# Kernel optimization log

Hardware: AMD Instinct MI355X
Metric: run time of the kernel (lower is better)

Reference implementation:

```python
import jax, jax.numpy as jnp
import numpy as np

B, D, H, E, TOP_K = 16384, 256, 1024, 8, 2


def setup_inputs() -> dict:
    key = jax.random.key(0)
    ks = jax.random.split(key, 12)
    s = 0.02
    return {
        "t": jax.random.uniform(ks[0], (B,), dtype=jnp.float32),
        "x": jax.random.normal(ks[1], (B, D), dtype=jnp.float32),
        # router: Linear(D+1,H) -> SiLU -> Linear(H,E)
        "Rw1": jax.random.normal(ks[2], (D + 1, H), dtype=jnp.float32) * s,
        "Rb1": jnp.zeros((H,), dtype=jnp.float32),
        "Rw2": jax.random.normal(ks[3], (H, E), dtype=jnp.float32) * s,
        "Rb2": jnp.zeros((E,), dtype=jnp.float32),
        # stacked expert MLPs: (D+1)->H->H->D for each of E experts
        "Ew1": jax.random.normal(ks[4], (E, D + 1, H), dtype=jnp.float32) * s,
        "Eb1": jnp.zeros((E, H), dtype=jnp.float32),
        "Ew2": jax.random.normal(ks[5], (E, H, H), dtype=jnp.float32) * s,
        "Eb2": jnp.zeros((E, H), dtype=jnp.float32),
        "Ew3": jax.random.normal(ks[6], (E, H, D), dtype=jnp.float32) * s,
        "Eb3": jnp.zeros((E, D), dtype=jnp.float32),
    }


def reference(t, x, Rw1, Rb1, Rw2, Rb2, Ew1, Eb1, Ew2, Eb2, Ew3, Eb3):
    t_vec = t.reshape(-1, 1)                      # (B,1)
    xt = jnp.concatenate([x, t_vec], axis=-1)     # (B,D+1)

    # router logits
    h = jax.nn.silu(xt @ Rw1 + Rb1)
    logits = h @ Rw2 + Rb2                        # (B,E)

    # top-k sparse gating (top_k < num_experts)
    topk_vals, topk_idx = jax.lax.top_k(logits, TOP_K)
    mask = jnp.zeros_like(logits).at[jnp.arange(logits.shape[0])[:, None], topk_idx].set(1.0)
    masked_logits = jnp.where(mask == 0, -jnp.inf, logits)
    alpha = jax.nn.softmax(masked_logits, axis=-1)  # (B,E)

    # dense all-expert MLPs (faithful to the original stack+einsum)
    h1 = jax.nn.silu(jnp.einsum('bi,eih->beh', xt, Ew1) + Eb1)   # (B,E,H)
    h2 = jax.nn.silu(jnp.einsum('beh,ehg->beg', h1, Ew2) + Eb2)  # (B,E,H)
    expert_out = jnp.einsum('beh,ehd->bed', h2, Ew3) + Eb3       # (B,E,D)

    velocity = jnp.einsum('be,bed->bd', alpha, expert_out)       # (B,D)
    return velocity
```

## Files before the change

kernel.cpp:

```cpp
#include <hip/hip_runtime.h>
#include <cstdint>
#include <cstddef>

#define NB   16384
#define DD   256
#define DIN  257
#define KP1  288
#define HH   1024
#define NE   8
#define GMAX 33792
#define GMT  264

#define CTRL_INTS 272

typedef unsigned short u16;
typedef __bf16 bf16x8 __attribute__((ext_vector_type(8)));
typedef float  f32x4  __attribute__((ext_vector_type(4)));
typedef unsigned short u16x4 __attribute__((ext_vector_type(4)));

__device__ __forceinline__ u16 f2bf(float f) {
  union { float f; unsigned u; } v; v.f = f;
  return (u16)((v.u + 0x7FFFu + ((v.u >> 16) & 1u)) >> 16);
}
__device__ __forceinline__ float bf2f(u16 h) {
  union { unsigned u; float f; } v; v.u = ((unsigned)h) << 16;
  return v.f;
}

#define GLDS16(g, l) __builtin_amdgcn_global_load_lds( \
    (const __attribute__((address_space(1))) void*)(g), \
    (__attribute__((address_space(3))) void*)(l), 16, 0, 0)

__device__ __forceinline__ int swz_u16(int row, int q) {
  return row * 32 + ((q ^ ((row >> 1) & 3)) * 8);
}

__global__ void build_xt3(const float* __restrict__ x, const float* __restrict__ t,
                          u16* __restrict__ xh, u16* __restrict__ xm, u16* __restrict__ xl) {
  long i = (long)blockIdx.x * 256 + threadIdx.x;
  int b = (int)(i / 72), qd = (int)(i % 72);
  f32x4 v;
  if (qd < 64)       v = *(const f32x4*)&x[(long)b * DD + qd * 4];
  else if (qd == 64) v = (f32x4){t[b], 0.f, 0.f, 0.f};
  else               v = (f32x4){0.f, 0.f, 0.f, 0.f};
  u16x4 h, m, l;
  #pragma unroll
  for (int j = 0; j < 4; ++j) {
    u16 hi = f2bf(v[j]);  float r1 = v[j] - bf2f(hi);
    u16 mi = f2bf(r1);    float r2 = r1 - bf2f(mi);
    h[j] = hi; m[j] = mi; l[j] = f2bf(r2);
  }
  long o = (long)b * KP1 + qd * 4;
  *(u16x4*)&xh[o] = h;  *(u16x4*)&xm[o] = m;  *(u16x4*)&xl[o] = l;
}

__global__ void transpose_all(const float* __restrict__ Rw1, const float* __restrict__ Ew1,
                              const float* __restrict__ Ew2, const float* __restrict__ Ew3,
                              u16* __restrict__ R1h, u16* __restrict__ R1m, u16* __restrict__ R1l,
                              u16* __restrict__ E1t, u16* __restrict__ E2t, u16* __restrict__ E3t) {
  __shared__ float tile[32][33];
  int bid = blockIdx.x;
  const float* W; u16 *Wh, *Wm = nullptr, *Wl = nullptr;
  int Kdim, Ndim, Kpad, e = 0, kt, nt;
  long sW = 0, sWt = 0;
  if (bid < 288) {
    kt = bid % 9; nt = bid / 9;
    W = Rw1; Wh = R1h; Wm = R1m; Wl = R1l; Kdim = DIN; Ndim = HH; Kpad = KP1;
  } else if (bid < 2592) {
    int b = bid - 288; e = b / 288; b %= 288; kt = b % 9; nt = b / 9;
    W = Ew1; Wh = E1t; Kdim = DIN; Ndim = HH; Kpad = KP1; sW = (long)DIN * HH; sWt = (long)HH * KP1;
  } else if (bid < 10784) {
    int b = bid - 2592; e = b / 1024; b %= 1024; kt = b % 32; nt = b / 32;
    W = Ew2; Wh = E2t; Kdim = HH; Ndim = HH; Kpad = HH; sW = (long)HH * HH; sWt = (long)HH * HH;
  } else {
    int b = bid - 10784; e = b / 256; b %= 256; kt = b % 32; nt = b / 32;
    W = Ew3; Wh = E3t; Kdim = HH; Ndim = DD; Kpad = HH; sW = (long)HH * DD; sWt = (long)DD * HH;
  }
  int k0 = kt * 32, n0 = nt * 32;
  int tx = threadIdx.x, ty = threadIdx.y;
  const float* Wb = W + (long)e * sW;
  #pragma unroll
  for (int i = 0; i < 4; ++i) {
    int k = k0 + ty + i * 8;
    tile[ty + i * 8][tx] = (k < Kdim) ? Wb[(long)k * Ndim + (n0 + tx)] : 0.f;
  }
  __syncthreads();
  #pragma unroll
  for (int i = 0; i < 4; ++i) {
    int n = n0 + ty + i * 8;
    float v = tile[tx][ty + i * 8];
    long o = (long)e * sWt + (long)n * Kpad + k0 + tx;
    u16 hi = f2bf(v);
    Wh[o] = hi;
    if (Wm) {
      float r1 = v - bf2f(hi);
      u16 mi = f2bf(r1);
      Wm[o] = mi;
      Wl[o] = f2bf(r1 - bf2f(mi));
    }
  }
}

__global__ __launch_bounds__(256, 2)
void router_gemm_emul3(const u16* __restrict__ Ah, const u16* __restrict__ Am, const u16* __restrict__ Al,
                       const u16* __restrict__ Bh, const u16* __restrict__ Bm, const u16* __restrict__ Bl,
                       const float* __restrict__ bias, const float* __restrict__ Rw2,
                       float* __restrict__ pbuf) {
  __shared__ __align__(16) u16 S[6][128 * 32];
  int tid = threadIdx.x;
  int bid = blockIdx.x;
  int xcd = bid & 7, j = bid >> 3;
  int mt = (j >> 3) * 8 + xcd, nt = j & 7;
  int m0 = mt * 128, n0 = nt * 128;
  const u16* Ap[3] = {Ah, Am, Al};
  const u16* Bp[3] = {Bh, Bm, Bl};
  const u16 *ag[3][2], *bg[3][2];
  u16 *la[3][2], *lb[3][2];
  #pragma unroll
  for (int r = 0; r < 2; ++r) {
    int i = r * 256 + tid;
    int row = i >> 2;
    int qa = (i & 3) ^ ((row >> 1) & 3);
    int kq = qa * 8;
    #pragma unroll
    for (int p = 0; p < 3; ++p) {
      ag[p][r] = Ap[p] + (long)(m0 + row) * KP1 + kq;
      bg[p][r] = Bp[p] + (long)(n0 + row) * KP1 + kq;
      la[p][r] = &S[p][i * 8];
      lb[p][r] = &S[3 + p][i * 8];
    }
  }
  int lane = tid & 63, wv = tid >> 6;
  int wm = wv >> 1, wn = wv & 1;
  int q = lane >> 4, c = lane & 15;
  int offA[4], offB[4];
  #pragma unroll
  for (int t4 = 0; t4 < 4; ++t4) {
    offA[t4] = swz_u16(wm * 64 + t4 * 16 + c, q);
    offB[t4] = swz_u16(wn * 64 + t4 * 16 + c, q);
  }
  f32x4 acc[4][4];
  #pragma unroll
  for (int mi = 0; mi < 4; ++mi)
    #pragma unroll
    for (int ni = 0; ni < 4; ++ni) acc[mi][ni] = (f32x4){0.f, 0.f, 0.f, 0.f};

  for (int k0 = 0; k0 < KP1; k0 += 32) {
    __syncthreads();
    #pragma unroll
    for (int r = 0; r < 2; ++r)
      #pragma unroll
      for (int p = 0; p < 3; ++p) {
        GLDS16(ag[p][r] + k0, la[p][r]);
        GLDS16(bg[p][r] + k0, lb[p][r]);
      }
    __syncthreads();
    bf16x8 av[3][4], bv[3][4];
    #pragma unroll
    for (int mi = 0; mi < 4; ++mi)
      #pragma unroll
      for (int p = 0; p < 3; ++p) av[p][mi] = *(const bf16x8*)&S[p][offA[mi]];
    #pragma unroll
    for (int ni = 0; ni < 4; ++ni)
      #pragma unroll
      for (int p = 0; p < 3; ++p) bv[p][ni] = *(const bf16x8*)&S[3 + p][offB[ni]];
    #pragma unroll
    for (int mi = 0; mi < 4; ++mi)
      #pragma unroll
      for (int ni = 0; ni < 4; ++ni) {
        acc[mi][ni] = __builtin_amdgcn_mfma_f32_16x16x32_bf16(av[0][mi], bv[0][ni], acc[mi][ni], 0, 0, 0);
        acc[mi][ni] = __builtin_amdgcn_mfma_f32_16x16x32_bf16(av[0][mi], bv[1][ni], acc[mi][ni], 0, 0, 0);
        acc[mi][ni] = __builtin_amdgcn_mfma_f32_16x16x32_bf16(av[1][mi], bv[0][ni], acc[mi][ni], 0, 0, 0);
        acc[mi][ni] = __builtin_amdgcn_mfma_f32_16x16x32_bf16(av[0][mi], bv[2][ni], acc[mi][ni], 0, 0, 0);
        acc[mi][ni] = __builtin_amdgcn_mfma_f32_16x16x32_bf16(av[2][mi], bv[0][ni], acc[mi][ni], 0, 0, 0);
      }
  }
  float rw2f[4][8];
  #pragma unroll
  for (int ni = 0; ni < 4; ++ni) {
    const float* p = Rw2 + (long)(n0 + wn * 64 + ni * 16 + c) * NE;
    f32x4 a = *(const f32x4*)p, b2 = *(const f32x4*)(p + 4);
    #pragma unroll
    for (int j2 = 0; j2 < 4; ++j2) { rw2f[ni][j2] = a[j2]; rw2f[ni][4 + j2] = b2[j2]; }
  }
  float bi[4];
  #pragma unroll
  for (int ni = 0; ni < 4; ++ni) bi[ni] = bias[n0 + wn * 64 + ni * 16 + c];
  #pragma unroll
  for (int mi = 0; mi < 4; ++mi)
    #pragma unroll
    for (int r = 0; r < 4; ++r) {
      int token = m0 + wm * 64 + mi * 16 + q * 4 + r;
      float part[8] = {0.f, 0.f, 0.f, 0.f, 0.f, 0.f, 0.f, 0.f};
      #pragma unroll
      for (int ni = 0; ni < 4; ++ni) {
        float v = acc[mi][ni][r] + bi[ni];
        v = v / (1.f + expf(-v));
        #pragma unroll
        for (int e = 0; e < 8; ++e) part[e] += v * rw2f[ni][e];
      }
      #pragma unroll
      for (int m = 1; m < 16; m <<= 1)
        #pragma unroll
        for (int e = 0; e < 8; ++e) part[e] += __shfl_xor(part[e], m, 64);
      if (c == 0) {
        float* dst = pbuf + ((long)(nt * 2 + wn) * NB + token) * 8;
        *(f32x4*)dst       = (f32x4){part[0], part[1], part[2], part[3]};
        *(f32x4*)(dst + 4) = (f32x4){part[4], part[5], part[6], part[7]};
      }
    }
}

__global__ void reduce_topk(const float* __restrict__ pbuf, const float* __restrict__ Rb2,
                            int* __restrict__ tk_idx, float* __restrict__ tk_alpha,
                            int* __restrict__ ctrl) {
  __shared__ int lh[NE];
  int tid = threadIdx.x;
  if (tid < NE) lh[tid] = 0;
  __syncthreads();
  int token = blockIdx.x * 256 + tid;
  float v[8];
  #pragma unroll
  for (int e = 0; e < 8; ++e) v[e] = Rb2[e];
  #pragma unroll
  for (int p = 0; p < 16; ++p) {
    const float* src = pbuf + ((long)p * NB + token) * 8;
    f32x4 a = *(const f32x4*)src, b = *(const f32x4*)(src + 4);
    #pragma unroll
    for (int j = 0; j < 4; ++j) { v[j] += a[j]; v[4 + j] += b[j]; }
  }
  int i0 = 0;
  #pragma unroll
  for (int e = 1; e < NE; ++e) if (v[e] > v[i0]) i0 = e;
  int i1 = -1;
  #pragma unroll
  for (int e = 0; e < NE; ++e) { if (e == i0) continue; if (i1 < 0 || v[e] > v[i1]) i1 = e; }
  float d  = v[i1] - v[i0];
  float e1 = expf(d);
  float a0 = 1.f / (1.f + e1);
  float a1 = e1 / (1.f + e1);
  tk_idx[token * 2]     = i0;  tk_idx[token * 2 + 1]   = i1;
  tk_alpha[token * 2]   = a0;  tk_alpha[token * 2 + 1] = a1;
  atomicAdd(&lh[i0], 1);  atomicAdd(&lh[i1], 1);
  __syncthreads();
  if (tid < NE) atomicAdd(&ctrl[tid * 16], lh[tid]);
  __syncthreads();
  if (tid == 0) {
    __threadfence();
    int done = atomicAdd(&ctrl[270], 1);
    if (done == gridDim.x - 1) {
      int total = 0;
      for (int e = 0; e < NE; ++e) {
        ctrl[256 + e] = total;
        total += (atomicAdd(&ctrl[e * 16], 0) + 127) & ~127;
      }
      ctrl[256 + NE] = total;
    }
  }
}

__global__ void build_rowmap(const int* __restrict__ tk_idx, int* __restrict__ ctrl,
                             int* __restrict__ grow, int* __restrict__ tok2slot) {
  __shared__ int lh[NE];
  __shared__ int gb[NE];
  int tid = threadIdx.x;
  if (tid < NE) lh[tid] = 0;
  __syncthreads();
  int token = blockIdx.x * 256 + tid;
  int e0 = tk_idx[token * 2], e1 = tk_idx[token * 2 + 1];
  int l0 = atomicAdd(&lh[e0], 1);
  int l1 = atomicAdd(&lh[e1], 1);
  __syncthreads();
  if (tid < NE) gb[tid] = atomicAdd(&ctrl[128 + tid * 16], lh[tid]);
  __syncthreads();
  int g0 = ctrl[256 + e0] + gb[e0] + l0;
  int g1 = ctrl[256 + e1] + gb[e1] + l1;
  grow[g0] = token;  grow[g1] = token;
  tok2slot[token * 2] = g0;  tok2slot[token * 2 + 1] = g1;
}

template<int NKT, int NT, int MINW, bool GATHER, bool SILU, bool OUTF32>
__global__ __launch_bounds__(256, MINW)
void gemm_grouped(const u16* __restrict__ A, int lda,
                  const u16* __restrict__ Wt, long wstride, int ldw,
                  const float* __restrict__ bias, int bstride,
                  u16* __restrict__ C, int ldc,
                  float* __restrict__ Out, int ldo,
                  const int* __restrict__ offp,
                  const int* __restrict__ grow,
                  int K) {
  int bid = blockIdx.x;
  int xcd = bid & 7, j = bid >> 3;
  int mt = (j / NT) * 8 + xcd, nt = j % NT;
  int m0 = mt * 128, n0 = nt * 128;
  if (m0 >= offp[NE]) return;
  int e = 0;
  while (m0 >= offp[e + 1]) ++e;
  __shared__ __align__(16) u16 As[NKT][128 * 32];
  __shared__ __align__(16) u16 Bs[NKT][128 * 32];
  int tid = threadIdx.x;
  const u16 *ag[NKT][2], *bg[NKT][2];
  u16 *la[NKT][2], *lb[NKT][2];
  #pragma unroll
  for (int s = 0; s < NKT; ++s)
    #pragma unroll
    for (int r = 0; r < 2; ++r) {
      int i = r * 256 + tid;
      int row = i >> 2;
      int qa = (i & 3) ^ ((row >> 1) & 3);
      int kq = qa * 8 + s * 32;
      long arow = m0 + row;
      if (GATHER) arow = grow[arow];
      ag[s][r] = A + arow * lda + kq;
      bg[s][r] = Wt + (long)e * wstride + (long)(n0 + row) * ldw + kq;
      la[s][r] = &As[s][i * 8];
      lb[s][r] = &Bs[s][i * 8];
    }
  int lane = tid & 63, wv = tid >> 6;
  int wm = wv >> 1, wn = wv & 1;
  int q = lane >> 4, c = lane & 15;
  int offA[4], offB[4];
  #pragma unroll
  for (int t4 = 0; t4 < 4; ++t4) {
    offA[t4] = swz_u16(wm * 64 + t4 * 16 + c, q);
    offB[t4] = swz_u16(wn * 64 + t4 * 16 + c, q);
  }
  f32x4 acc[4][4];
  #pragma unroll
  for (int mi = 0; mi < 4; ++mi)
    #pragma unroll
    for (int ni = 0; ni < 4; ++ni) acc[mi][ni] = (f32x4){0.f, 0.f, 0.f, 0.f};

  for (int k0 = 0; k0 < K; k0 += 32 * NKT) {
    __syncthreads();
    #pragma unroll
    for (int s = 0; s < NKT; ++s)
      #pragma unroll
      for (int r = 0; r < 2; ++r) {
        GLDS16(ag[s][r] + k0, la[s][r]);
        GLDS16(bg[s][r] + k0, lb[s][r]);
      }
    __syncthreads();
    #pragma unroll
    for (int s = 0; s < NKT; ++s) {
      bf16x8 av[4], bv[4];
      #pragma unroll
      for (int mi = 0; mi < 4; ++mi)
        av[mi] = *(const bf16x8*)&As[s][offA[mi]];
      #pragma unroll
      for (int ni = 0; ni < 4; ++ni)
        bv[ni] = *(const bf16x8*)&Bs[s][offB[ni]];
      #pragma unroll
      for (int mi = 0; mi < 4; ++mi)
        #pragma unroll
        for (int ni = 0; ni < 4; ++ni)
          acc[mi][ni] = __builtin_amdgcn_mfma_f32_16x16x32_bf16(av[mi], bv[ni], acc[mi][ni], 0, 0, 0);
    }
  }
  #pragma unroll
  for (int mi = 0; mi < 4; ++mi)
    #pragma unroll
    for (int r = 0; r < 4; ++r) {
      int row = wm * 64 + mi * 16 + q * 4 + r;
      #pragma unroll
      for (int ni = 0; ni < 4; ++ni) {
        int col = n0 + wn * 64 + ni * 16 + c;
        float v = acc[mi][ni][r] + bias[e * bstride + col];
        if constexpr (SILU) v = v / (1.f + __expf(-v));
        if constexpr (OUTF32) {
          Out[(long)(m0 + row) * ldo + col] = v;
        } else {
          C[(long)(m0 + row) * ldc + col] = f2bf(v);
        }
      }
    }
}

__global__ void combine_out(const float* __restrict__ eo, const int* __restrict__ tok2slot,
                            const float* __restrict__ tk_alpha, float* __restrict__ out) {
  int i = blockIdx.x * 256 + threadIdx.x;
  int token = i >> 6, c4 = (i & 63) * 4;
  long s0 = tok2slot[token * 2], s1 = tok2slot[token * 2 + 1];
  float a0 = tk_alpha[token * 2], a1 = tk_alpha[token * 2 + 1];
  f32x4 v0 = *(const f32x4*)&eo[s0 * DD + c4];
  f32x4 v1 = *(const f32x4*)&eo[s1 * DD + c4];
  f32x4 r;
  #pragma unroll
  for (int j = 0; j < 4; ++j) r[j] = a0 * v0[j] + a1 * v1[j];
  *(f32x4*)&out[(long)token * DD + c4] = r;
}

extern "C" void kernel_launch(void* const* d_in, const int* in_sizes, int n_in,
                              void* d_out, int out_size, void* d_ws, size_t ws_size,
                              hipStream_t stream) {
  const float* t   = (const float*)d_in[0];
  const float* x   = (const float*)d_in[1];
  const float* Rw1 = (const float*)d_in[2];
  const float* Rb1 = (const float*)d_in[3];
  const float* Rw2 = (const float*)d_in[4];
  const float* Rb2 = (const float*)d_in[5];
  const float* Ew1 = (const float*)d_in[6];
  const float* Eb1 = (const float*)d_in[7];
  const float* Ew2 = (const float*)d_in[8];
  const float* Eb2 = (const float*)d_in[9];
  const float* Ew3 = (const float*)d_in[10];
  const float* Eb3 = (const float*)d_in[11];
  float* out = (float*)d_out;

  char* w = (char*)d_ws;
  size_t off = 0;
  auto alloc = [&](size_t bytes) { char* p = w + off; off = (off + bytes + 255) & ~(size_t)255; return p; };
  int*   ctrl     = (int*)  alloc(CTRL_INTS * 4);
  int*   grow     = (int*)  alloc((size_t)GMAX * 4);
  size_t zero_end = off;
  int*   tok2slot = (int*)  alloc((size_t)NB * 2 * 4);
  int*   tk_idx   = (int*)  alloc((size_t)NB * 2 * 4);
  float* tk_alpha = (float*)alloc((size_t)NB * 2 * 4);
  float* pbuf     = (float*)alloc((size_t)16 * NB * 8 * 4);
  u16* xh  = (u16*)alloc((size_t)NB * KP1 * 2);
  u16* xm  = (u16*)alloc((size_t)NB * KP1 * 2);
  u16* xl  = (u16*)alloc((size_t)NB * KP1 * 2);
  u16* R1h = (u16*)alloc((size_t)HH * KP1 * 2);
  u16* R1m = (u16*)alloc((size_t)HH * KP1 * 2);
  u16* R1l = (u16*)alloc((size_t)HH * KP1 * 2);
  u16* E1t = (u16*)alloc((size_t)NE * HH * KP1 * 2);
  u16* E2t = (u16*)alloc((size_t)NE * HH * HH * 2);
  u16* E3t = (u16*)alloc((size_t)NE * DD * HH * 2);
  u16* H1  = (u16*)alloc((size_t)GMAX * HH * 2);
  u16* H2  = (u16*)alloc((size_t)GMAX * HH * 2);
  float* eo = (float*)H1;

  hipMemsetAsync(d_ws, 0, zero_end, stream);

  build_xt3<<<(NB * 72) / 256, 256, 0, stream>>>(x, t, xh, xm, xl);
  transpose_all<<<12832, dim3(32, 8), 0, stream>>>(Rw1, Ew1, Ew2, Ew3,
                                                   R1h, R1m, R1l, E1t, E2t, E3t);

  router_gemm_emul3<<<(NB / 128) * 8, 256, 0, stream>>>(xh, xm, xl, R1h, R1m, R1l, Rb1, Rw2, pbuf);
  reduce_topk<<<NB / 256, 256, 0, stream>>>(pbuf, Rb2, tk_idx, tk_alpha, ctrl);
  build_rowmap<<<NB / 256, 256, 0, stream>>>(tk_idx, ctrl, grow, tok2slot);

  const int* offp = ctrl + 256;
  gemm_grouped<3, 8, 3, true, true, false><<<GMT * 8, 256, 0, stream>>>(
      xh, KP1, E1t, (long)HH * KP1, KP1, Eb1, HH, H1, HH, nullptr, 0, offp, grow, KP1);
  gemm_grouped<2, 8, 4, false, true, false><<<GMT * 8, 256, 0, stream>>>(
      H1, HH, E2t, (long)HH * HH, HH, Eb2, HH, H2, HH, nullptr, 0, offp, nullptr, HH);
  gemm_grouped<2, 2, 4, false, false, true><<<GMT * 2, 256, 0, stream>>>(
      H2, HH, E3t, (long)DD * HH, HH, Eb3, DD, nullptr, 0, eo, DD, offp, nullptr, HH);
  combine_out<<<(NB * DD / 4) / 256, 256, 0, stream>>>(eo, tok2slot, tk_alpha, out);
}
```

Measured before the change: 398.6 us.

## Fuse preprocessing kernels, split-K the final expert GEMM, parallelize top-k reduction

```diff
diff --git a/kernel.cpp b/kernel.cpp
--- a/kernel.cpp
+++ b/kernel.cpp
@@ -35,31 +35,35 @@
   return row * 32 + ((q ^ ((row >> 1) & 3)) * 8);
 }
 
-__global__ void build_xt3(const float* __restrict__ x, const float* __restrict__ t,
-                          u16* __restrict__ xh, u16* __restrict__ xm, u16* __restrict__ xl) {
-  long i = (long)blockIdx.x * 256 + threadIdx.x;
-  int b = (int)(i / 72), qd = (int)(i % 72);
-  f32x4 v;
-  if (qd < 64)       v = *(const f32x4*)&x[(long)b * DD + qd * 4];
-  else if (qd == 64) v = (f32x4){t[b], 0.f, 0.f, 0.f};
-  else               v = (f32x4){0.f, 0.f, 0.f, 0.f};
-  u16x4 h, m, l;
-  #pragma unroll
-  for (int j = 0; j < 4; ++j) {
-    u16 hi = f2bf(v[j]);  float r1 = v[j] - bf2f(hi);
-    u16 mi = f2bf(r1);    float r2 = r1 - bf2f(mi);
-    h[j] = hi; m[j] = mi; l[j] = f2bf(r2);
-  }
-  long o = (long)b * KP1 + qd * 4;
-  *(u16x4*)&xh[o] = h;  *(u16x4*)&xm[o] = m;  *(u16x4*)&xl[o] = l;
-}
-
-__global__ void transpose_all(const float* __restrict__ Rw1, const float* __restrict__ Ew1,
-                              const float* __restrict__ Ew2, const float* __restrict__ Ew3,
-                              u16* __restrict__ R1h, u16* __restrict__ R1m, u16* __restrict__ R1l,
-                              u16* __restrict__ E1t, u16* __restrict__ E2t, u16* __restrict__ E3t) {
+#define XT_BLOCKS 4608
+__global__ void preprocess(const float* __restrict__ x, const float* __restrict__ t,
+                           u16* __restrict__ xh, u16* __restrict__ xm, u16* __restrict__ xl,
+                           const float* __restrict__ Rw1, const float* __restrict__ Ew1,
+                           const float* __restrict__ Ew2, const float* __restrict__ Ew3,
+                           u16* __restrict__ R1h, u16* __restrict__ R1m, u16* __restrict__ R1l,
+                           u16* __restrict__ E1t, u16* __restrict__ E2t, u16* __restrict__ E3t) {
   __shared__ float tile[32][33];
+  int tid = threadIdx.x;
   int bid = blockIdx.x;
+  if (bid < XT_BLOCKS) {
+    long i = (long)bid * 256 + tid;
+    int b = (int)(i / 72), qd = (int)(i % 72);
+    f32x4 v;
+    if (qd < 64)       v = *(const f32x4*)&x[(long)b * DD + qd * 4];
+    else if (qd == 64) v = (f32x4){t[b], 0.f, 0.f, 0.f};
+    else               v = (f32x4){0.f, 0.f, 0.f, 0.f};
+    u16x4 h, m, l;
+    #pragma unroll
+    for (int j = 0; j < 4; ++j) {
+      u16 hi = f2bf(v[j]);  float r1 = v[j] - bf2f(hi);
+      u16 mi = f2bf(r1);    float r2 = r1 - bf2f(mi);
+      h[j] = hi; m[j] = mi; l[j] = f2bf(r2);
+    }
+    long o = (long)b * KP1 + qd * 4;
+    *(u16x4*)&xh[o] = h;  *(u16x4*)&xm[o] = m;  *(u16x4*)&xl[o] = l;
+    return;
+  }
+  bid -= XT_BLOCKS;
   const float* W; u16 *Wh, *Wm = nullptr, *Wl = nullptr;
   int Kdim, Ndim, Kpad, e = 0, kt, nt;
   long sW = 0, sWt = 0;
@@ -77,7 +81,7 @@
     W = Ew3; Wh = E3t; Kdim = HH; Ndim = DD; Kpad = HH; sW = (long)HH * DD; sWt = (long)DD * HH;
   }
   int k0 = kt * 32, n0 = nt * 32;
-  int tx = threadIdx.x, ty = threadIdx.y;
+  int tx = tid & 31, ty = tid >> 5;
   const float* Wb = W + (long)e * sW;
   #pragma unroll
   for (int i = 0; i < 4; ++i) {
@@ -218,30 +222,38 @@
   int tid = threadIdx.x;
   if (tid < NE) lh[tid] = 0;
   __syncthreads();
-  int token = blockIdx.x * 256 + tid;
-  float v[8];
-  #pragma unroll
-  for (int e = 0; e < 8; ++e) v[e] = Rb2[e];
-  #pragma unroll
-  for (int p = 0; p < 16; ++p) {
+  int gi = blockIdx.x * 256 + tid;
+  int token = gi >> 2, sub = gi & 3;
+  float v[8] = {0.f, 0.f, 0.f, 0.f, 0.f, 0.f, 0.f, 0.f};
+  #pragma unroll
+  for (int pp = 0; pp < 4; ++pp) {
+    int p = sub * 4 + pp;
     const float* src = pbuf + ((long)p * NB + token) * 8;
     f32x4 a = *(const f32x4*)src, b = *(const f32x4*)(src + 4);
     #pragma unroll
     for (int j = 0; j < 4; ++j) { v[j] += a[j]; v[4 + j] += b[j]; }
   }
-  int i0 = 0;
-  #pragma unroll
-  for (int e = 1; e < NE; ++e) if (v[e] > v[i0]) i0 = e;
-  int i1 = -1;
-  #pragma unroll
-  for (int e = 0; e < NE; ++e) { if (e == i0) continue; if (i1 < 0 || v[e] > v[i1]) i1 = e; }
-  float d  = v[i1] - v[i0];
-  float e1 = expf(d);
-  float a0 = 1.f / (1.f + e1);
-  float a1 = e1 / (1.f + e1);
-  tk_idx[token * 2]     = i0;  tk_idx[token * 2 + 1]   = i1;
-  tk_alpha[token * 2]   = a0;  tk_alpha[token * 2 + 1] = a1;
-  atomicAdd(&lh[i0], 1);  atomicAdd(&lh[i1], 1);
+  #pragma unroll
+  for (int m = 1; m < 4; m <<= 1)
+    #pragma unroll
+    for (int e = 0; e < NE; ++e) v[e] += __shfl_xor(v[e], m, 64);
+  if (sub == 0) {
+    #pragma unroll
+    for (int e = 0; e < NE; ++e) v[e] += Rb2[e];
+    int i0 = 0;
+    #pragma unroll
+    for (int e = 1; e < NE; ++e) if (v[e] > v[i0]) i0 = e;
+    int i1 = -1;
+    #pragma unroll
+    for (int e = 0; e < NE; ++e) { if (e == i0) continue; if (i1 < 0 || v[e] > v[i1]) i1 = e; }
+    float d  = v[i1] - v[i0];
+    float e1 = expf(d);
+    float a0 = 1.f / (1.f + e1);
+    float a1 = e1 / (1.f + e1);
+    tk_idx[token * 2]     = i0;  tk_idx[token * 2 + 1]   = i1;
+    tk_alpha[token * 2]   = a0;  tk_alpha[token * 2 + 1] = a1;
+    atomicAdd(&lh[i0], 1);  atomicAdd(&lh[i1], 1);
+  }
   __syncthreads();
   if (tid < NE) atomicAdd(&ctrl[tid * 16], lh[tid]);
   __syncthreads();
@@ -279,7 +291,7 @@
   tok2slot[token * 2] = g0;  tok2slot[token * 2 + 1] = g1;
 }
 
-template<int NKT, int NT, int MINW, bool GATHER, bool SILU, bool OUTF32>
+template<int NKT, int NT, int KS, int MINW, bool GATHER, bool SILU, bool OUTF32>
 __global__ __launch_bounds__(256, MINW)
 void gemm_grouped(const u16* __restrict__ A, int lda,
                   const u16* __restrict__ Wt, long wstride, int ldw,
@@ -291,7 +303,8 @@
                   int K) {
   int bid = blockIdx.x;
   int xcd = bid & 7, j = bid >> 3;
-  int mt = (j / NT) * 8 + xcd, nt = j % NT;
+  int nt = j % NT, ks = (j / NT) % KS;
+  int mt = (j / (NT * KS)) * 8 + xcd;
   int m0 = mt * 128, n0 = nt * 128;
   if (m0 >= offp[NE]) return;
   int e = 0;
@@ -331,7 +344,8 @@
     #pragma unroll
     for (int ni = 0; ni < 4; ++ni) acc[mi][ni] = (f32x4){0.f, 0.f, 0.f, 0.f};
 
-  for (int k0 = 0; k0 < K; k0 += 32 * NKT) {
+  int kbeg = ks * (K / KS), kend = (ks + 1) * (K / KS);
+  for (int k0 = kbeg; k0 < kend; k0 += 32 * NKT) {
     __syncthreads();
     #pragma unroll
     for (int s = 0; s < NKT; ++s)
@@ -357,6 +371,7 @@
           acc[mi][ni] = __builtin_amdgcn_mfma_f32_16x16x32_bf16(av[mi], bv[ni], acc[mi][ni], 0, 0, 0);
     }
   }
+  float* OutP = Out + (long)ks * GMAX * ldo;
   #pragma unroll
   for (int mi = 0; mi < 4; ++mi)
     #pragma unroll
@@ -365,10 +380,11 @@
       #pragma unroll
       for (int ni = 0; ni < 4; ++ni) {
         int col = n0 + wn * 64 + ni * 16 + c;
-        float v = acc[mi][ni][r] + bias[e * bstride + col];
+        float bv2 = (KS == 1 || ks == 0) ? bias[e * bstride + col] : 0.f;
+        float v = acc[mi][ni][r] + bv2;
         if constexpr (SILU) v = v / (1.f + __expf(-v));
         if constexpr (OUTF32) {
-          Out[(long)(m0 + row) * ldo + col] = v;
+          OutP[(long)(m0 + row) * ldo + col] = v;
         } else {
           C[(long)(m0 + row) * ldc + col] = f2bf(v);
         }
@@ -382,11 +398,14 @@
   int token = i >> 6, c4 = (i & 63) * 4;
   long s0 = tok2slot[token * 2], s1 = tok2slot[token * 2 + 1];
   float a0 = tk_alpha[token * 2], a1 = tk_alpha[token * 2 + 1];
-  f32x4 v0 = *(const f32x4*)&eo[s0 * DD + c4];
-  f32x4 v1 = *(const f32x4*)&eo[s1 * DD + c4];
+  const float* eo1 = eo + (long)GMAX * DD;
+  f32x4 v0a = *(const f32x4*)&eo[s0 * DD + c4];
+  f32x4 v0b = *(const f32x4*)&eo1[s0 * DD + c4];
+  f32x4 v1a = *(const f32x4*)&eo[s1 * DD + c4];
+  f32x4 v1b = *(const f32x4*)&eo1[s1 * DD + c4];
   f32x4 r;
   #pragma unroll
-  for (int j = 0; j < 4; ++j) r[j] = a0 * v0[j] + a1 * v1[j];
+  for (int j = 0; j < 4; ++j) r[j] = a0 * (v0a[j] + v0b[j]) + a1 * (v1a[j] + v1b[j]);
   *(f32x4*)&out[(long)token * DD + c4] = r;
 }
 
@@ -432,20 +451,20 @@
 
   hipMemsetAsync(d_ws, 0, zero_end, stream);
 
-  build_xt3<<<(NB * 72) / 256, 256, 0, stream>>>(x, t, xh, xm, xl);
-  transpose_all<<<12832, dim3(32, 8), 0, stream>>>(Rw1, Ew1, Ew2, Ew3,
-                                                   R1h, R1m, R1l, E1t, E2t, E3t);
+  preprocess<<<XT_BLOCKS + 12832, 256, 0, stream>>>(x, t, xh, xm, xl,
+                                                    Rw1, Ew1, Ew2, Ew3,
+                                                    R1h, R1m, R1l, E1t, E2t, E3t);
 
   router_gemm_emul3<<<(NB / 128) * 8, 256, 0, stream>>>(xh, xm, xl, R1h, R1m, R1l, Rb1, Rw2, pbuf);
-  reduce_topk<<<NB / 256, 256, 0, stream>>>(pbuf, Rb2, tk_idx, tk_alpha, ctrl);
+  reduce_topk<<<(NB * 4) / 256, 256, 0, stream>>>(pbuf, Rb2, tk_idx, tk_alpha, ctrl);
   build_rowmap<<<NB / 256, 256, 0, stream>>>(tk_idx, ctrl, grow, tok2slot);
 
   const int* offp = ctrl + 256;
-  gemm_grouped<3, 8, 3, true, true, false><<<GMT * 8, 256, 0, stream>>>(
+  gemm_grouped<3, 8, 1, 3, true, true, false><<<GMT * 8, 256, 0, stream>>>(
       xh, KP1, E1t, (long)HH * KP1, KP1, Eb1, HH, H1, HH, nullptr, 0, offp, grow, KP1);
-  gemm_grouped<2, 8, 4, false, true, false><<<GMT * 8, 256, 0, stream>>>(
+  gemm_grouped<2, 8, 1, 4, false, true, false><<<GMT * 8, 256, 0, stream>>>(
       H1, HH, E2t, (long)HH * HH, HH, Eb2, HH, H2, HH, nullptr, 0, offp, nullptr, HH);
-  gemm_grouped<2, 2, 4, false, false, true><<<GMT * 2, 256, 0, stream>>>(
+  gemm_grouped<2, 2, 2, 4, false, false, true><<<GMT * 2 * 2, 256, 0, stream>>>(
       H2, HH, E3t, (long)DD * HH, HH, Eb3, DD, nullptr, 0, eo, DD, offp, nullptr, HH);
   combine_out<<<(NB * DD / 4) / 256, 256, 0, stream>>>(eo, tok2slot, tk_alpha, out);
 }
```

New measurement: 428.4 us. +7.5%, slower.
